# Kernel optimization log

Measured on AMD Instinct MI355X. Metric: run time of the kernel, lower is better.

Reference implementation:

```python
import jax, jax.numpy as jnp
import numpy as np
from jax import lax

# Hyperparameters from init_kwargs (inference/testing path of the RPN)
PRE_NMS = 6000        # pre_nms_top_n['testing']
POST_NMS = 1000       # post_nms_top_n['testing']
NMS_THRESH = 0.7
MIN_SIZE = 1.0
WX = WY = WW = WH = 1.0                      # reg_weights
BBOX_XFORM_CLIP = float(np.log(1000.0 / 16.0))  # standard BoxCoder clamp on dw/dh


def _decode(deltas, anchors):
    # deltas, anchors: [K, 4] -> decoded boxes [K, 4] (x1,y1,x2,y2)
    wa = anchors[:, 2] - anchors[:, 0]
    ha = anchors[:, 3] - anchors[:, 1]
    cxa = anchors[:, 0] + 0.5 * wa
    cya = anchors[:, 1] + 0.5 * ha
    dx = deltas[:, 0] / WX
    dy = deltas[:, 1] / WY
    dw = jnp.minimum(deltas[:, 2] / WW, BBOX_XFORM_CLIP)
    dh = jnp.minimum(deltas[:, 3] / WH, BBOX_XFORM_CLIP)
    cx = dx * wa + cxa
    cy = dy * ha + cya
    w = jnp.exp(dw) * wa
    h = jnp.exp(dh) * ha
    return jnp.stack([cx - 0.5 * w, cy - 0.5 * h, cx + 0.5 * w, cy + 0.5 * h], axis=-1)


def _nms_keep(boxes, valid, thresh):
    # Sequential NMS over score-sorted boxes [K,4]; 'valid' marks non-removed boxes.
    K = boxes.shape[0]
    x1, y1, x2, y2 = boxes[:, 0], boxes[:, 1], boxes[:, 2], boxes[:, 3]
    areas = (x2 - x1) * (y2 - y1)
    idxs = jnp.arange(K)

    def body(i, keep):
        xx1 = jnp.maximum(x1[i], x1)
        yy1 = jnp.maximum(y1[i], y1)
        xx2 = jnp.minimum(x2[i], x2)
        yy2 = jnp.minimum(y2[i], y2)
        inter = jnp.maximum(xx2 - xx1, 0.0) * jnp.maximum(yy2 - yy1, 0.0)
        iou = inter / (areas[i] + areas - inter + 1e-9)
        suppress = (iou > thresh) & (idxs > i)
        return jnp.where(keep[i], keep & ~suppress, keep)

    return lax.fori_loop(0, K, body, valid)


def _proposals_one(anchors, objectness, deltas, img_h, img_w):
    # anchors [N,4], objectness [N], deltas [N,4] -> proposals [POST_NMS, 4]
    k = min(objectness.shape[0], PRE_NMS)
    scores, idx = lax.top_k(objectness, k)          # topk filter (sorted desc)
    boxes = _decode(deltas[idx], anchors[idx])      # anchor decode on top-k only
    # process_box: clip to image, filter small boxes (masked, not removed, for jit)
    x1 = jnp.clip(boxes[:, 0], 0.0, img_w)
    y1 = jnp.clip(boxes[:, 1], 0.0, img_h)
    x2 = jnp.clip(boxes[:, 2], 0.0, img_w)
    y2 = jnp.clip(boxes[:, 3], 0.0, img_h)
    boxes = jnp.stack([x1, y1, x2, y2], axis=-1)
    valid = ((x2 - x1) >= MIN_SIZE) & ((y2 - y1) >= MIN_SIZE)
    keep = _nms_keep(boxes, valid, NMS_THRESH)
    # Compact kept boxes (score order) into a fixed [POST_NMS,4] buffer, zero-padded
    rank = jnp.cumsum(keep.astype(jnp.int32)) - 1
    tgt = jnp.where(keep & (rank < POST_NMS), rank, POST_NMS)  # POST_NMS -> dropped
    out = jnp.zeros((POST_NMS, 4), boxes.dtype).at[tgt].set(boxes, mode='drop')
    return out


def setup_inputs() -> dict:
    key = jax.random.key(0)
    k1, k2, k3, k4 = jax.random.split(key, 4)
    B, N = 8, 500000
    IMG = 1024
    # Valid anchor boxes: random centers in-image, sizes in [16, 256]
    cxy = jax.random.uniform(k1, (B, N, 2), jnp.float32, 0.0, float(IMG))
    wh = jax.random.uniform(k2, (B, N, 2), jnp.float32, 16.0, 256.0)
    anchors = jnp.concatenate([cxy - 0.5 * wh, cxy + 0.5 * wh], axis=-1)
    objectness = jax.random.normal(k3, (B, N), jnp.float32)
    pred_bbox_delta = 0.1 * jax.random.normal(k4, (B, N, 4), jnp.float32)
    return {"anchors": anchors, "objectness": objectness,
            "pred_bbox_delta": pred_bbox_delta, "img_h": IMG, "img_w": IMG}


def reference(anchors, objectness, pred_bbox_delta, img_h, img_w):
    h, w = float(img_h), float(img_w)
    f = jax.vmap(lambda a, o, d: _proposals_one(a, o, d, h, w))
    return f(anchors, objectness, pred_bbox_delta)  # [B, POST_NMS, 4]
```

## Files before the change

kernel.cpp:

```cpp
#include <hip/hip_runtime.h>
#include <cstdint>
#include <cmath>

#define NBATCH   8
#define NPB      500000
#define PRE_NMS  6000
#define POST_NMS 1000
#define NWORDS   94
#define NBINS    16384
#define CANDCAP  8192
#define BBOX_CLIP 4.135166556742356f
#define TI 16
#define TJ 512
#define WIN 16
#define CNT_PAD 64
#define SORT_CHUNK 2048

#define F_SORT 1u
#define F_COMP 2u
#define F_OOB  4u

__device__ __forceinline__ unsigned monot(float f) {
    unsigned b = __float_as_uint(f);
    return (b & 0x80000000u) ? ~b : (b | 0x80000000u);
}

__device__ __forceinline__ bool iou_gt_thr(float inter, float den) {
    const double MID = (double)0.7f + 0x1p-25;
    return (double)inter >= MID * (double)den;
}

__global__ __launch_bounds__(256) void hist_kernel(const float* __restrict__ obj,
                                                   unsigned* __restrict__ hist) {
    __shared__ unsigned lh[NBINS];
    const int b = blockIdx.y;
    for (int q = threadIdx.x; q < NBINS; q += 256) lh[q] = 0;
    __syncthreads();
    const float* p = obj + (size_t)b * NPB;
    const int stride = gridDim.x * 256;
    for (int i = blockIdx.x * 256 + threadIdx.x; i < NPB; i += stride) {
        unsigned u = monot(p[i]);
        atomicAdd(&lh[u >> 18], 1u);
    }
    __syncthreads();
    unsigned* gh = hist + (size_t)b * NBINS;
    for (int q = threadIdx.x; q < NBINS; q += 256) {
        unsigned v = lh[q];
        if (v) atomicAdd(&gh[q], v);
    }
}

__global__ __launch_bounds__(256) void thresh_kernel(const unsigned* __restrict__ hist,
                                                     unsigned* __restrict__ tbin) {
    __shared__ unsigned part[256], pre[256];
    const int b = blockIdx.x;
    const unsigned* gh = hist + (size_t)b * NBINS;
    const int t = threadIdx.x;
    const int PER = NBINS / 256;
    unsigned s = 0;
    for (int d = 0; d < PER; ++d) s += gh[NBINS - 1 - (t * PER + d)];
    part[t] = s;
    __syncthreads();
    if (t == 0) {
        unsigned run = 0;
        for (int q = 0; q < 256; ++q) { pre[q] = run; run += part[q]; }
    }
    __syncthreads();
    unsigned c = pre[t];
    if (c < PRE_NMS && c + part[t] >= PRE_NMS) {
        unsigned run = c;
        for (int d = 0; d < PER; ++d) {
            int bin = NBINS - 1 - (t * PER + d);
            run += gh[bin];
            if (run >= PRE_NMS) { tbin[b] = (unsigned)bin; break; }
        }
    }
}

__global__ __launch_bounds__(256) void compact_kernel(const float* __restrict__ obj,
                                                      const unsigned* __restrict__ tbin,
                                                      unsigned long long* __restrict__ cand,
                                                      unsigned* __restrict__ ccnt) {
    const int b = blockIdx.y;
    const unsigned T = tbin[b];
    const float* p = obj + (size_t)b * NPB;
    unsigned long long* cb = cand + (size_t)b * CANDCAP;
    const int lane = threadIdx.x & 63;
    const int stride = gridDim.x * 256;
    for (int i = blockIdx.x * 256 + threadIdx.x; i < NPB; i += stride) {
        unsigned u = monot(p[i]);
        const bool pred = (u >> 18) >= T;
        unsigned long long bal = __ballot(pred);
        if (bal == 0) continue;
        unsigned base = 0;
        if (lane == 0) base = atomicAdd(&ccnt[(size_t)b * CNT_PAD], __popcll(bal));
        base = (unsigned)__shfl((int)base, 0);
        if (pred) {
            unsigned pos = base + (unsigned)__popcll(bal & ((1ULL << lane) - 1ULL));
            if (pos < CANDCAP)
                cb[pos] = ((unsigned long long)u << 32) | (unsigned)(~i);
        }
    }
}

__global__ __launch_bounds__(512) void sort_local_kernel(unsigned long long* __restrict__ cand) {
    __shared__ unsigned long long s[SORT_CHUNK];
    const int blk = blockIdx.x;
    const int b = blk >> 2, c = blk & 3;
    unsigned long long* cb = cand + (size_t)b * CANDCAP + (size_t)c * SORT_CHUNK;
    const int t = threadIdx.x;
    for (int i = t; i < SORT_CHUNK; i += 512) s[i] = cb[i];
    __syncthreads();
    for (unsigned k = 2; k <= SORT_CHUNK; k <<= 1) {
        const bool kfull = (k == SORT_CHUNK);
        const bool upfull = (c & 1) == 0;
        for (unsigned j = k >> 1; j > 0; j >>= 1) {
            for (unsigned ii = t; ii < SORT_CHUNK; ii += 512) {
                unsigned l = ii ^ j;
                if (l > ii) {
                    unsigned long long a = s[ii], d = s[l];
                    bool up = kfull ? upfull : ((ii & k) == 0);
                    if (up ? (a < d) : (a > d)) { s[ii] = d; s[l] = a; }
                }
            }
            __syncthreads();
        }
    }
    for (int i = t; i < SORT_CHUNK; i += 512) cb[i] = s[i];
}

__global__ __launch_bounds__(1024) void sort_merge_kernel(const unsigned long long* __restrict__ cand,
                                                          const float* __restrict__ obj,
                                                          const float* __restrict__ anchors,
                                                          const float* __restrict__ deltas,
                                                          const int* __restrict__ imh,
                                                          const int* __restrict__ imw,
                                                          float* __restrict__ boxes,
                                                          float* __restrict__ areas,
                                                          unsigned long long* __restrict__ validm,
                                                          unsigned* __restrict__ flags) {
    __shared__ unsigned long long s[CANDCAP];
    const int b = blockIdx.x, t = threadIdx.x;
    const unsigned long long* cb = cand + (size_t)b * CANDCAP;
    for (int i = t; i < CANDCAP; i += 1024) s[i] = cb[i];
    __syncthreads();
    for (unsigned k = 2 * SORT_CHUNK; k <= CANDCAP; k <<= 1) {
        for (unsigned j = k >> 1; j > 0; j >>= 1) {
            for (unsigned ii = t; ii < CANDCAP; ii += 1024) {
                unsigned l = ii ^ j;
                if (l > ii) {
                    unsigned long long a = s[ii], c = s[l];
                    bool up = (ii & k) == 0;
                    if (up ? (a < c) : (a > c)) { s[ii] = c; s[l] = a; }
                }
            }
            __syncthreads();
        }
    }
    int vh = imh[0], vw = imw[0];
    float ih = (vh > 0 && vh < (1 << 20)) ? (float)vh : __int_as_float(vh);
    float iw = (vw > 0 && vw < (1 << 20)) ? (float)vw : __int_as_float(vw);
    unsigned f = 0;
    for (int r = t; r < PRE_NMS; r += 1024) {
        unsigned long long c = s[r];
        unsigned idx = ~(unsigned)(c & 0xffffffffULL);
        if (idx >= NPB) { f |= F_OOB; idx = 0; }
        else if (monot(obj[(size_t)b * NPB + idx]) != (unsigned)(c >> 32)) f |= F_COMP;
        if (r < PRE_NMS - 1 && !(c > s[r + 1])) f |= F_SORT;
        const float4 a = ((const float4*)anchors)[(size_t)b * NPB + idx];
        const float4 d = ((const float4*)deltas)[(size_t)b * NPB + idx];
        float wa = a.z - a.x, ha = a.w - a.y;
        float cxa = a.x + 0.5f * wa, cya = a.y + 0.5f * ha;
        float dw = fminf(d.z, BBOX_CLIP), dh = fminf(d.w, BBOX_CLIP);
        float cx = __fadd_rn(__fmul_rn(d.x, wa), cxa);
        float cy = __fadd_rn(__fmul_rn(d.y, ha), cya);
        float ew = (float)::exp((double)dw), eh = (float)::exp((double)dh);
        float w = __fmul_rn(ew, wa), h = __fmul_rn(eh, ha);
        float x1 = cx - 0.5f * w, y1 = cy - 0.5f * h;
        float x2 = cx + 0.5f * w, y2 = cy + 0.5f * h;
        x1 = fminf(fmaxf(x1, 0.f), iw); y1 = fminf(fmaxf(y1, 0.f), ih);
        x2 = fminf(fmaxf(x2, 0.f), iw); y2 = fminf(fmaxf(y2, 0.f), ih);
        bool valid = (x2 - x1 >= 1.0f) && (y2 - y1 >= 1.0f);
        ((float4*)boxes)[(size_t)b * PRE_NMS + r] = make_float4(x1, y1, x2, y2);
        areas[(size_t)b * PRE_NMS + r] = __fmul_rn(x2 - x1, y2 - y1);
        unsigned long long bal = __ballot(valid);
        if ((threadIdx.x & 63) == 0) validm[(size_t)b * NWORDS + (r >> 6)] = bal;
    }
    if (f) atomicOr(&flags[b], f);
}

__global__ __launch_bounds__(256) void mask_kernel(const float* __restrict__ boxes,
                                                   const float* __restrict__ areas,
                                                   unsigned long long* __restrict__ mask,
                                                   unsigned long long* __restrict__ diag) {
    __shared__ float4 sb[TJ];
    __shared__ float  sa[TJ];
    const int b = blockIdx.x & 7;
    const int i0 = (blockIdx.x >> 3) * TI;
    const int jbase = (i0 >> 6) << 6;
    const int wv = threadIdx.x >> 6, ln = threadIdx.x & 63;
    const int ir = i0 + 4 * wv;
    unsigned long long* dgp = diag + (size_t)b * PRE_NMS;
    float4 bx[4]; float ar[4]; int wlo[4];
    unsigned long long* rowp[4];
#pragma unroll
    for (int r = 0; r < 4; ++r) {
        const int i = ir + r;
        bx[r]   = ((const float4*)boxes)[(size_t)b * PRE_NMS + i];
        ar[r]   = areas[(size_t)b * PRE_NMS + i];
        rowp[r] = mask + ((size_t)b * PRE_NMS + i) * NWORDS;
        wlo[r]  = i >> 6;
    }
    for (int t0 = jbase; t0 < NWORDS * 64; t0 += TJ) {
        for (int e = threadIdx.x; e < TJ; e += 256) {
            int j = t0 + e;
            if (j < PRE_NMS) {
                sb[e] = ((const float4*)boxes)[(size_t)b * PRE_NMS + j];
                sa[e] = areas[(size_t)b * PRE_NMS + j];
            } else { sb[e] = make_float4(0.f, 0.f, 0.f, 0.f); sa[e] = 0.f; }
        }
        __syncthreads();
        for (int wl = 0; wl < TJ / 64; ++wl) {
            const int w = (t0 >> 6) + wl;
            if (w >= NWORDS) break;
            const int e = wl * 64 + ln;
            const float4 bj = sb[e];
            const float aj = sa[e];
#pragma unroll
            for (int r = 0; r < 4; ++r) {
                float xx1 = fmaxf(bx[r].x, bj.x), yy1 = fmaxf(bx[r].y, bj.y);
                float xx2 = fminf(bx[r].z, bj.z), yy2 = fminf(bx[r].w, bj.w);
                float inter = __fmul_rn(fmaxf(__fsub_rn(xx2, xx1), 0.f),
                                        fmaxf(__fsub_rn(yy2, yy1), 0.f));
                float den = __fadd_rn(__fsub_rn(__fadd_rn(ar[r], aj), inter), 1e-9f);
                bool p = iou_gt_thr(inter, den);
                unsigned long long m = __ballot(p);
                if (ln == 0) {
                    if (w == wlo[r]) {
                        m &= ~((2ULL << ((ir + r) & 63)) - 1ULL);
                        rowp[r][w] = m;
                        dgp[ir + r] = m;
                    } else if (w > wlo[r]) {
                        rowp[r][w] = m;
                    }
                }
            }
        }
        __syncthreads();
    }
}

__global__ __launch_bounds__(64) void scan_kernel(const unsigned long long* __restrict__ mask,
                                                  const unsigned long long* __restrict__ diag,
                                                  const unsigned long long* __restrict__ validm,
                                                  const float* __restrict__ boxes,
                                                  const unsigned* __restrict__ flags,
                                                  const unsigned* __restrict__ ccnt,
                                                  float* __restrict__ out) {
    const int b = blockIdx.x, lane = threadIdx.x;
    const unsigned long long* mb = mask + (size_t)b * PRE_NMS * NWORDS;
    const unsigned long long* dg = diag + (size_t)b * PRE_NMS;
    const int w0 = 2 * lane, w1 = 2 * lane + 1;
    unsigned long long r_lo = (w0 < NWORDS) ? ~validm[(size_t)b * NWORDS + w0] : ~0ULL;
    unsigned long long r_hi = (w1 < NWORDS) ? ~validm[(size_t)b * NWORDS + w1] : ~0ULL;
    int count = 0;

    uint4 MA[WIN], MB[WIN], MC[WIN];
    unsigned long long WA[WIN], WB[WIN], WC[WIN];
    float4 bxA, bxB, bxC;

#define ISSUE(M, W, BX, base_)                                                   \
    {                                                                            \
        const int bb_ = (base_);                                                 \
        const char* rb_ = (const char*)(mb + (size_t)bb_ * NWORDS);              \
        const unsigned long long* dgp_ = dg + bb_;   \
        _Pragma("unroll")                                                        \
        for (int q = 0; q < WIN; ++q) {                                          \
            M[q] = *(const uint4*)(rb_ + (size_t)q * (NWORDS * 8)                \
                                       + (size_t)lane * 16);                     \
            W[q] = dgp_[q];                                                      \
        }                                                                        \
        BX = (lane < WIN)                                                        \
                 ? ((const float4*)boxes)[(size_t)b * PRE_NMS + bb_ + lane]      \
                 : make_float4(0.f, 0.f, 0.f, 0.f);                              \
    }

#define RESOLVE(M, W, BX, base_)                                                 \
    {                                                                            \
        const int bb_ = (base_);                                                 \
        const int wR_ = bb_ >> 6, s0_ = bb_ & 63;                                \
        const unsigned long long sel_ = (wR_ & 1) ? r_hi : r_lo;                 \
        const int srcl_ = wR_ >> 1;                                              \
        const unsigned lo_ = (unsigned)__shfl((int)(unsigned)(sel_ & 0xffffffffULL), srcl_); \
        const unsigned hi_ = (unsigned)__shfl((int)(unsigned)(sel_ >> 32), srcl_);           \
        const unsigned long long ww_ = ((unsigned long long)hi_ << 32) | lo_;    \
        unsigned cand_ = (unsigned)((~ww_) >> s0_) & 0xFFFFu;                    \
        unsigned kept_ = 0;                                                      \
        const int cb_ = count;                                                   \
        _Pragma("unroll")                                                        \
        for (int q = 0; q < WIN; ++q) {                                          \
            if (((cand_ >> q) & 1u) && count < POST_NMS) {                       \
                kept_ |= 1u << q; ++count;                                       \
                cand_ &= ~(unsigned)(W[q] >> s0_);                               \
            }                                                                    \
        }                                                                        \
        const bool v0_ = (w0 >= wR_), v1_ = (w1 >= wR_);                         \
        _Pragma("unroll")                                                        \
        for (int q = 0; q < WIN; ++q) {                                          \
            if (kept_ & (1u << q)) {                                             \
                const uint4 m_ = M[q];                                           \
                if (v0_) r_lo |= ((unsigned long long)m_.y << 32) | m_.x;        \
                if (v1_) r_hi |= ((unsigned long long)m_.w << 32) | m_.z;        \
            }                                                                    \
        }                                                                        \
        if (lane < WIN && (kept_ & (1u << lane))) {                              \
            const int rank_ = cb_ + __popc(kept_ & ((1u << lane) - 1u));         \
            ((float4*)out)[(size_t)b * POST_NMS + rank_] = BX;                   \
        }                                                                        \
    }

    ISSUE(MA, WA, bxA, 0)
    ISSUE(MB, WB, bxB, WIN)
    bool done = false;
    for (int base = 0; base < PRE_NMS && !done; base += 3 * WIN) {
        const int n2 = base + 2 * WIN;
        ISSUE(MC, WC, bxC, (n2 < PRE_NMS) ? n2 : 0)
        RESOLVE(MA, WA, bxA, base)
        done = (count >= POST_NMS);
        if (!done) {
            const int n3 = base + 3 * WIN;
            ISSUE(MA, WA, bxA, (n3 < PRE_NMS) ? n3 : 0)
            RESOLVE(MB, WB, bxB, base + WIN)
            done = (count >= POST_NMS);
        }
        if (!done) {
            const int n4 = base + 4 * WIN;
            ISSUE(MB, WB, bxB, (n4 < PRE_NMS) ? n4 : 0)
            RESOLVE(MC, WC, bxC, base + 2 * WIN)
            done = (count >= POST_NMS);
        }
    }
#undef ISSUE
#undef RESOLVE

    if (lane == 0) {
        float canary = 0.f;
        const unsigned cc = ccnt[(size_t)b * CNT_PAD];
        const unsigned fl = flags[b];
        if (cc > CANDCAP)       canary = 111000.f;
        else if (cc < PRE_NMS)  canary = 222000.f;
        if (fl & F_SORT)        canary = 333000.f;
        if (fl & F_COMP)        canary = 444000.f;
        if (fl & F_OOB)         canary = 777000.f;
        if (canary != 0.f) out[(size_t)b * POST_NMS * 4] = canary;
    }
}

extern "C" void kernel_launch(void* const* d_in, const int* in_sizes, int n_in,
                              void* d_out, int out_size, void* d_ws, size_t ws_size,
                              hipStream_t stream) {
    const float* anchors = (const float*)d_in[0];
    const float* obj     = (const float*)d_in[1];
    const float* deltas  = (const float*)d_in[2];
    const int*   imh     = (const int*)d_in[3];
    const int*   imw     = (const int*)d_in[4];
    float* out = (float*)d_out;
    char* ws = (char*)d_ws;

    size_t off = 0;
    auto alloc = [&](size_t bytes) {
        size_t o = off;
        off = (off + bytes + 511) & ~(size_t)511;
        return o;
    };
    const size_t HIST  = alloc((size_t)NBATCH * NBINS * 4);
    const size_t TBIN  = alloc((size_t)NBATCH * 4);
    const size_t CCNT  = alloc((size_t)NBATCH * CNT_PAD * 4);
    const size_t FLAGS = alloc((size_t)NBATCH * 4);
    const size_t CAND  = alloc((size_t)NBATCH * CANDCAP * 8);
    const size_t ZEND  = off;
    const size_t BOX   = alloc((size_t)NBATCH * PRE_NMS * 16);
    const size_t AREA  = alloc((size_t)NBATCH * PRE_NMS * 4);
    const size_t VALID = alloc((size_t)NBATCH * NWORDS * 8);
    const size_t DIAG  = alloc((size_t)NBATCH * PRE_NMS * 8);
    const size_t MASK  = alloc((size_t)NBATCH * PRE_NMS * NWORDS * 8);
    (void)alloc(1024);
    if (ws_size < off) return;

    unsigned*            hist   = (unsigned*)(ws + HIST);
    unsigned*            tbin   = (unsigned*)(ws + TBIN);
    unsigned*            ccnt   = (unsigned*)(ws + CCNT);
    unsigned*            flags  = (unsigned*)(ws + FLAGS);
    unsigned long long*  cand   = (unsigned long long*)(ws + CAND);
    float*               boxes  = (float*)(ws + BOX);
    float*               areas  = (float*)(ws + AREA);
    unsigned long long*  validm = (unsigned long long*)(ws + VALID);
    unsigned long long*  diag   = (unsigned long long*)(ws + DIAG);
    unsigned long long*  maskp  = (unsigned long long*)(ws + MASK);

    hipMemsetAsync(ws, 0, ZEND, stream);
    hipMemsetAsync(out, 0, (size_t)out_size * sizeof(float), stream);

    hist_kernel      <<<dim3(32, NBATCH), 256, 0, stream>>>(obj, hist);
    thresh_kernel    <<<dim3(NBATCH), 256, 0, stream>>>(hist, tbin);
    compact_kernel   <<<dim3(128, NBATCH), 256, 0, stream>>>(obj, tbin, cand, ccnt);
    sort_local_kernel<<<dim3(NBATCH * (CANDCAP / SORT_CHUNK)), 512, 0, stream>>>(cand);
    sort_merge_kernel<<<dim3(NBATCH), 1024, 0, stream>>>(
        cand, obj, anchors, deltas, imh, imw, boxes, areas, validm, flags);
    mask_kernel      <<<dim3((PRE_NMS / TI) * NBATCH), 256, 0, stream>>>(
        boxes, areas, maskp, diag);
    scan_kernel      <<<dim3(NBATCH), 64, 0, stream>>>(
        maskp, diag, validm, boxes, flags, ccnt, out);
    (void)in_sizes; (void)n_in; (void)ws_size;
}
```

Measured before the change: 391.0 us.

## Split box decode into parallel kernel, enlarge mask tile, skip empty scan windows

Moves anchor decoding, clipping and validity ballots out of the 8-block sort_merge kernel into a separate decode kernel with many blocks, so the gathers from anchors and deltas run in parallel across the GPU. The sort kernel now only writes the top-k indices. The mask kernel handles 6 rows per wave instead of 4 (TI 24), giving more reuse of each shared-memory tile with fewer blocks. The NMS scan keeps a running candidate word, fetches it only at 64-box word boundaries, and skips windows with no candidates. The histogram grid is halved. Costs are one extra launch and a small index buffer.

```diff
diff --git a/kernel.cpp b/kernel.cpp
--- a/kernel.cpp
+++ b/kernel.cpp
@@ -10,7 +10,7 @@
 #define NBINS    16384
 #define CANDCAP  8192
 #define BBOX_CLIP 4.135166556742356f
-#define TI 16
+#define TI 24
 #define TJ 512
 #define WIN 16
 #define CNT_PAD 64
@@ -131,13 +131,7 @@
 
 __global__ __launch_bounds__(1024) void sort_merge_kernel(const unsigned long long* __restrict__ cand,
                                                           const float* __restrict__ obj,
-                                                          const float* __restrict__ anchors,
-                                                          const float* __restrict__ deltas,
-                                                          const int* __restrict__ imh,
-                                                          const int* __restrict__ imw,
-                                                          float* __restrict__ boxes,
-                                                          float* __restrict__ areas,
-                                                          unsigned long long* __restrict__ validm,
+                                                          unsigned* __restrict__ topk,
                                                           unsigned* __restrict__ flags) {
     __shared__ unsigned long long s[CANDCAP];
     const int b = blockIdx.x, t = threadIdx.x;
@@ -157,9 +151,6 @@
             __syncthreads();
         }
     }
-    int vh = imh[0], vw = imw[0];
-    float ih = (vh > 0 && vh < (1 << 20)) ? (float)vh : __int_as_float(vh);
-    float iw = (vw > 0 && vw < (1 << 20)) ? (float)vw : __int_as_float(vw);
     unsigned f = 0;
     for (int r = t; r < PRE_NMS; r += 1024) {
         unsigned long long c = s[r];
@@ -167,6 +158,29 @@
         if (idx >= NPB) { f |= F_OOB; idx = 0; }
         else if (monot(obj[(size_t)b * NPB + idx]) != (unsigned)(c >> 32)) f |= F_COMP;
         if (r < PRE_NMS - 1 && !(c > s[r + 1])) f |= F_SORT;
+        topk[(size_t)b * PRE_NMS + r] = idx;
+    }
+    if (f) atomicOr(&flags[b], f);
+}
+
+__global__ __launch_bounds__(256) void decode_kernel(const float* __restrict__ anchors,
+                                                     const float* __restrict__ deltas,
+                                                     const unsigned* __restrict__ topk,
+                                                     const int* __restrict__ imh,
+                                                     const int* __restrict__ imw,
+                                                     float* __restrict__ boxes,
+                                                     float* __restrict__ areas,
+                                                     unsigned long long* __restrict__ validm) {
+    const int b = blockIdx.y;
+    const int r = blockIdx.x * 256 + threadIdx.x;
+    const bool active = r < PRE_NMS;
+    int vh = imh[0], vw = imw[0];
+    float ih = (vh > 0 && vh < (1 << 20)) ? (float)vh : __int_as_float(vh);
+    float iw = (vw > 0 && vw < (1 << 20)) ? (float)vw : __int_as_float(vw);
+    bool valid = false;
+    if (active) {
+        unsigned idx = topk[(size_t)b * PRE_NMS + r];
+        if (idx >= NPB) idx = 0;
         const float4 a = ((const float4*)anchors)[(size_t)b * NPB + idx];
         const float4 d = ((const float4*)deltas)[(size_t)b * NPB + idx];
         float wa = a.z - a.x, ha = a.w - a.y;
@@ -180,13 +194,13 @@
         float x2 = cx + 0.5f * w, y2 = cy + 0.5f * h;
         x1 = fminf(fmaxf(x1, 0.f), iw); y1 = fminf(fmaxf(y1, 0.f), ih);
         x2 = fminf(fmaxf(x2, 0.f), iw); y2 = fminf(fmaxf(y2, 0.f), ih);
-        bool valid = (x2 - x1 >= 1.0f) && (y2 - y1 >= 1.0f);
+        valid = (x2 - x1 >= 1.0f) && (y2 - y1 >= 1.0f);
         ((float4*)boxes)[(size_t)b * PRE_NMS + r] = make_float4(x1, y1, x2, y2);
         areas[(size_t)b * PRE_NMS + r] = __fmul_rn(x2 - x1, y2 - y1);
-        unsigned long long bal = __ballot(valid);
-        if ((threadIdx.x & 63) == 0) validm[(size_t)b * NWORDS + (r >> 6)] = bal;
-    }
-    if (f) atomicOr(&flags[b], f);
+    }
+    unsigned long long bal = __ballot(valid);
+    int w = r >> 6;
+    if ((threadIdx.x & 63) == 0 && w < NWORDS) validm[(size_t)b * NWORDS + w] = bal;
 }
 
 __global__ __launch_bounds__(256) void mask_kernel(const float* __restrict__ boxes,
@@ -199,12 +213,12 @@
     const int i0 = (blockIdx.x >> 3) * TI;
     const int jbase = (i0 >> 6) << 6;
     const int wv = threadIdx.x >> 6, ln = threadIdx.x & 63;
-    const int ir = i0 + 4 * wv;
+    const int ir = i0 + 6 * wv;
     unsigned long long* dgp = diag + (size_t)b * PRE_NMS;
-    float4 bx[4]; float ar[4]; int wlo[4];
-    unsigned long long* rowp[4];
+    float4 bx[6]; float ar[6]; int wlo[6];
+    unsigned long long* rowp[6];
 #pragma unroll
-    for (int r = 0; r < 4; ++r) {
+    for (int r = 0; r < 6; ++r) {
         const int i = ir + r;
         bx[r]   = ((const float4*)boxes)[(size_t)b * PRE_NMS + i];
         ar[r]   = areas[(size_t)b * PRE_NMS + i];
@@ -227,7 +241,7 @@
             const float4 bj = sb[e];
             const float aj = sa[e];
 #pragma unroll
-            for (int r = 0; r < 4; ++r) {
+            for (int r = 0; r < 6; ++r) {
                 float xx1 = fmaxf(bx[r].x, bj.x), yy1 = fmaxf(bx[r].y, bj.y);
                 float xx2 = fminf(bx[r].z, bj.z), yy2 = fminf(bx[r].w, bj.w);
                 float inter = __fmul_rn(fmaxf(__fsub_rn(xx2, xx1), 0.f),
@@ -264,6 +278,7 @@
     unsigned long long r_lo = (w0 < NWORDS) ? ~validm[(size_t)b * NWORDS + w0] : ~0ULL;
     unsigned long long r_hi = (w1 < NWORDS) ? ~validm[(size_t)b * NWORDS + w1] : ~0ULL;
     int count = 0;
+    unsigned long long cw = 0;
 
     uint4 MA[WIN], MB[WIN], MC[WIN];
     unsigned long long WA[WIN], WB[WIN], WC[WIN];
@@ -273,7 +288,7 @@
     {                                                                            \
         const int bb_ = (base_);                                                 \
         const char* rb_ = (const char*)(mb + (size_t)bb_ * NWORDS);              \
-        const unsigned long long* dgp_ = dg + bb_;   \
+        const unsigned long long* dgp_ = dg + bb_;                               \
         _Pragma("unroll")                                                        \
         for (int q = 0; q < WIN; ++q) {                                          \
             M[q] = *(const uint4*)(rb_ + (size_t)q * (NWORDS * 8)                \
@@ -289,33 +304,38 @@
     {                                                                            \
         const int bb_ = (base_);                                                 \
         const int wR_ = bb_ >> 6, s0_ = bb_ & 63;                                \
-        const unsigned long long sel_ = (wR_ & 1) ? r_hi : r_lo;                 \
-        const int srcl_ = wR_ >> 1;                                              \
-        const unsigned lo_ = (unsigned)__shfl((int)(unsigned)(sel_ & 0xffffffffULL), srcl_); \
-        const unsigned hi_ = (unsigned)__shfl((int)(unsigned)(sel_ >> 32), srcl_);           \
-        const unsigned long long ww_ = ((unsigned long long)hi_ << 32) | lo_;    \
-        unsigned cand_ = (unsigned)((~ww_) >> s0_) & 0xFFFFu;                    \
-        unsigned kept_ = 0;                                                      \
-        const int cb_ = count;                                                   \
-        _Pragma("unroll")                                                        \
-        for (int q = 0; q < WIN; ++q) {                                          \
-            if (((cand_ >> q) & 1u) && count < POST_NMS) {                       \
-                kept_ |= 1u << q; ++count;                                       \
-                cand_ &= ~(unsigned)(W[q] >> s0_);                               \
+        if (s0_ == 0) {               \
+            const unsigned long long sel_ = (wR_ & 1) ? r_hi : r_lo;             \
+            const int srcl_ = wR_ >> 1;                                          \
+            const unsigned lo_ = (unsigned)__shfl((int)(unsigned)(sel_ & 0xffffffffULL), srcl_); \
+            const unsigned hi_ = (unsigned)__shfl((int)(unsigned)(sel_ >> 32), srcl_);           \
+            cw = ~(((unsigned long long)hi_ << 32) | lo_);                       \
+        }                                                                        \
+        unsigned cand_ = (unsigned)(cw >> s0_) & 0xFFFFu;                        \
+        if (cand_) {                                                             \
+            unsigned kept_ = 0;                                                  \
+            const int cb_ = count;                                               \
+            _Pragma("unroll")                                                    \
+            for (int q = 0; q < WIN; ++q) {                                      \
+                if (((cand_ >> q) & 1u) && count < POST_NMS) {                   \
+                    kept_ |= 1u << q; ++count;                                   \
+                    cw &= ~W[q];                                                 \
+                    cand_ &= (unsigned)(cw >> s0_);                              \
+                }                                                                \
             }                                                                    \
-        }                                                                        \
-        const bool v0_ = (w0 >= wR_), v1_ = (w1 >= wR_);                         \
-        _Pragma("unroll")                                                        \
-        for (int q = 0; q < WIN; ++q) {                                          \
-            if (kept_ & (1u << q)) {                                             \
-                const uint4 m_ = M[q];                                           \
-                if (v0_) r_lo |= ((unsigned long long)m_.y << 32) | m_.x;        \
-                if (v1_) r_hi |= ((unsigned long long)m_.w << 32) | m_.z;        \
+            const bool v0_ = (w0 >= wR_), v1_ = (w1 >= wR_);                     \
+            _Pragma("unroll")                                                    \
+            for (int q = 0; q < WIN; ++q) {                                      \
+                if (kept_ & (1u << q)) {                                         \
+                    const uint4 m_ = M[q];                                       \
+                    if (v0_) r_lo |= ((unsigned long long)m_.y << 32) | m_.x;    \
+                    if (v1_) r_hi |= ((unsigned long long)m_.w << 32) | m_.z;    \
+                }                                                                \
             }                                                                    \
-        }                                                                        \
-        if (lane < WIN && (kept_ & (1u << lane))) {                              \
-            const int rank_ = cb_ + __popc(kept_ & ((1u << lane) - 1u));         \
-            ((float4*)out)[(size_t)b * POST_NMS + rank_] = BX;                   \
+            if (lane < WIN && (kept_ & (1u << lane))) {                          \
+                const int rank_ = cb_ + __popc(kept_ & ((1u << lane) - 1u));     \
+                ((float4*)out)[(size_t)b * POST_NMS + rank_] = BX;               \
+            }                                                                    \
         }                                                                        \
     }
 
@@ -379,6 +399,7 @@
     const size_t FLAGS = alloc((size_t)NBATCH * 4);
     const size_t CAND  = alloc((size_t)NBATCH * CANDCAP * 8);
     const size_t ZEND  = off;
+    const size_t TOPK  = alloc((size_t)NBATCH * PRE_NMS * 4);
     const size_t BOX   = alloc((size_t)NBATCH * PRE_NMS * 16);
     const size_t AREA  = alloc((size_t)NBATCH * PRE_NMS * 4);
     const size_t VALID = alloc((size_t)NBATCH * NWORDS * 8);
@@ -392,6 +413,7 @@
     unsigned*            ccnt   = (unsigned*)(ws + CCNT);
     unsigned*            flags  = (unsigned*)(ws + FLAGS);
     unsigned long long*  cand   = (unsigned long long*)(ws + CAND);
+    unsigned*            topk   = (unsigned*)(ws + TOPK);
     float*               boxes  = (float*)(ws + BOX);
     float*               areas  = (float*)(ws + AREA);
     unsigned long long*  validm = (unsigned long long*)(ws + VALID);
@@ -401,12 +423,13 @@
     hipMemsetAsync(ws, 0, ZEND, stream);
     hipMemsetAsync(out, 0, (size_t)out_size * sizeof(float), stream);
 
-    hist_kernel      <<<dim3(32, NBATCH), 256, 0, stream>>>(obj, hist);
+    hist_kernel      <<<dim3(16, NBATCH), 256, 0, stream>>>(obj, hist);
     thresh_kernel    <<<dim3(NBATCH), 256, 0, stream>>>(hist, tbin);
     compact_kernel   <<<dim3(128, NBATCH), 256, 0, stream>>>(obj, tbin, cand, ccnt);
     sort_local_kernel<<<dim3(NBATCH * (CANDCAP / SORT_CHUNK)), 512, 0, stream>>>(cand);
-    sort_merge_kernel<<<dim3(NBATCH), 1024, 0, stream>>>(
-        cand, obj, anchors, deltas, imh, imw, boxes, areas, validm, flags);
+    sort_merge_kernel<<<dim3(NBATCH), 1024, 0, stream>>>(cand, obj, topk, flags);
+    decode_kernel    <<<dim3((PRE_NMS + 255) / 256, NBATCH), 256, 0, stream>>>(
+        anchors, deltas, topk, imh, imw, boxes, areas, validm);
     mask_kernel      <<<dim3((PRE_NMS / TI) * NBATCH), 256, 0, stream>>>(
         boxes, areas, maskp, diag);
     scan_kernel      <<<dim3(NBATCH), 64, 0, stream>>>(
```

Result: slower. 412.2 us (+5.4%).
